# Kernel optimization log

Hardware: AMD Instinct MI355X
Metric: run time of the kernel (lower is better)

The kernel has to match this reference:

```python
import jax, jax.numpy as jnp
import numpy as np

N_LAYER = 3
N_HEAD = 12
D_K = 64
D_V = 64
D_MODEL = 768
D_INNER = 4096
LN_EPS = 1e-5
BN_EPS = 1e-5
PAD_ID = 1


def _layernorm(x, g, b):
    m = jnp.mean(x, axis=-1, keepdims=True)
    v = jnp.mean((x - m) ** 2, axis=-1, keepdims=True)
    return g * (x - m) / jnp.sqrt(v + LN_EPS) + b


def _batchnorm(x, g, b):
    # training-mode BatchNorm1d: per-feature batch statistics
    m = jnp.mean(x, axis=0)
    v = jnp.mean((x - m) ** 2, axis=0)
    return g * (x - m) / jnp.sqrt(v + BN_EPS) + b


def setup_inputs() -> dict:
    key = jax.random.key(0)
    ks = jax.random.split(key, 24)
    B, C, S, H = 4, 4, 256, D_MODEL
    inp = {
        'input_ids': jax.random.randint(ks[0], (B, C, S), 0, 50000, dtype=jnp.int64) if jax.config.read('jax_enable_x64') else jax.random.randint(ks[0], (B, C, S), 0, 50000, dtype=jnp.int32),
        'roberta_attn': jax.random.normal(ks[1], (B, C, S, H), dtype=jnp.float32),
        'pooled_output': jax.random.normal(ks[2], (B * C, H), dtype=jnp.float32),
        'commonsense_mask': jax.random.uniform(ks[3], (B, C, S, S), dtype=jnp.float32),
        'dependency_mask': jax.random.uniform(ks[4], (B, C, S, S), dtype=jnp.float32),
        'entity_mask': jax.random.uniform(ks[5], (B, C, S), dtype=jnp.float32),
        'sentiment_mask': jax.random.uniform(ks[6], (B, C, S, S), dtype=jnp.float32),
    }
    s = 0.02
    inp['lin_w'] = s * jax.random.normal(ks[7], (H, N_LAYER * 4), dtype=jnp.float32)
    inp['lin_b'] = jnp.zeros((N_LAYER * 4,), jnp.float32)
    inp['Wq'] = s * jax.random.normal(ks[8], (N_LAYER, H, N_HEAD * D_K), dtype=jnp.float32)
    inp['bq'] = jnp.zeros((N_LAYER, N_HEAD * D_K), jnp.float32)
    inp['Wk'] = s * jax.random.normal(ks[9], (N_LAYER, H, N_HEAD * D_K), dtype=jnp.float32)
    inp['bk'] = jnp.zeros((N_LAYER, N_HEAD * D_K), jnp.float32)
    inp['Wv'] = s * jax.random.normal(ks[10], (N_LAYER, H, N_HEAD * D_V), dtype=jnp.float32)
    inp['bv'] = jnp.zeros((N_LAYER, N_HEAD * D_V), jnp.float32)
    inp['Wo'] = s * jax.random.normal(ks[11], (N_LAYER, N_HEAD * D_V, H), dtype=jnp.float32)
    inp['bo'] = jnp.zeros((N_LAYER, H), jnp.float32)
    inp['ln1_g'] = jnp.ones((N_LAYER, H), jnp.float32)
    inp['ln1_b'] = jnp.zeros((N_LAYER, H), jnp.float32)
    inp['W1'] = s * jax.random.normal(ks[12], (N_LAYER, H, D_INNER), dtype=jnp.float32)
    inp['b1'] = jnp.zeros((N_LAYER, D_INNER), jnp.float32)
    inp['W2'] = s * jax.random.normal(ks[13], (N_LAYER, D_INNER, H), dtype=jnp.float32)
    inp['b2'] = jnp.zeros((N_LAYER, H), jnp.float32)
    inp['ln2_g'] = jnp.ones((N_LAYER, H), jnp.float32)
    inp['ln2_b'] = jnp.zeros((N_LAYER, H), jnp.float32)
    inp['bnt_g'] = jnp.ones((H,), jnp.float32)
    inp['bnt_b'] = jnp.zeros((H,), jnp.float32)
    inp['pool_w'] = s * jax.random.normal(ks[14], (H, H), dtype=jnp.float32)
    inp['pool_b'] = jnp.zeros((H,), jnp.float32)
    inp['bn_g'] = jnp.ones((H,), jnp.float32)
    inp['bn_b'] = jnp.zeros((H,), jnp.float32)
    inp['cls_w'] = s * jax.random.normal(ks[15], (H, 1), dtype=jnp.float32)
    inp['cls_b'] = jnp.zeros((1,), jnp.float32)
    return inp


def reference(input_ids, roberta_attn, pooled_output, commonsense_mask, dependency_mask,
              entity_mask, sentiment_mask, lin_w, lin_b, Wq, bq, Wk, bk, Wv, bv, Wo, bo,
              ln1_g, ln1_b, W1, b1, W2, b2, ln2_g, ln2_b, bnt_g, bnt_b,
              pool_w, pool_b, bn_g, bn_b, cls_w, cls_b):
    B, C, S = input_ids.shape
    H = roberta_attn.shape[-1]
    N = B * C
    x = roberta_attn.reshape(N, S, H)

    # learned softmax fusion weights over the 4 relational masks, per layer
    w = jnp.mean(x, axis=1) @ lin_w + lin_b                       # [N, 3*4]
    w = jax.nn.softmax(w.reshape(N, N_LAYER, 4).transpose(1, 0, 2), axis=-1)  # [3, N, 4]

    ent = jnp.broadcast_to(entity_mask[:, :, None, :], (B, C, S, S))
    masks = jnp.stack([
        commonsense_mask.reshape(N, S, S),
        dependency_mask.reshape(N, S, S),
        ent.reshape(N, S, S),
        sentiment_mask.reshape(N, S, S),
    ], axis=1)                                                     # [N, 4, S, S]
    bias = jnp.einsum('lnm,nmqk->lnqk', w, masks)                  # [3, N, S, S]

    non_pad = (input_ids.reshape(N, S) != PAD_ID).astype(x.dtype)[:, :, None]  # [N, S, 1]

    enc = x
    scale = 1.0 / np.sqrt(D_K).astype(np.float32)
    for l in range(N_LAYER):
        residual = enc
        q = (enc @ Wq[l] + bq[l]).reshape(N, S, N_HEAD, D_K)
        k = (enc @ Wk[l] + bk[l]).reshape(N, S, N_HEAD, D_K)
        v = (enc @ Wv[l] + bv[l]).reshape(N, S, N_HEAD, D_V)
        scores = jnp.einsum('nqhd,nkhd->nhqk', q, k) * scale + bias[l][:, None]  # [N,H,S,S]
        attn = jax.nn.softmax(scores, axis=-1)
        o = jnp.einsum('nhqk,nkhd->nqhd', attn, v).reshape(N, S, N_HEAD * D_V)
        o = o @ Wo[l] + bo[l]
        enc = _layernorm(o + residual, ln1_g[l], ln1_b[l]) * non_pad
        residual = enc
        f = jax.nn.relu(enc @ W1[l] + b1[l]) @ W2[l] + b2[l]
        enc = _layernorm(f + residual, ln2_g[l], ln2_b[l]) * non_pad

    enc = _batchnorm(enc.reshape(N * S, H), bnt_g, bnt_b).reshape(N, S, H)
    seq = x + enc
    pooled = jnp.tanh(seq[:, 0] @ pool_w + pool_b)
    pooled = _batchnorm(pooled, bn_g, bn_b)
    logits = pooled @ cls_w + cls_b                                # [N, 1]
    return logits.reshape(-1, C)
```

## Files before the change

kernel.cpp:

```cpp
#include <hip/hip_runtime.h>
#include <hip/hip_bf16.h>
#include <math.h>

#define NSEQ 16
#define SEQ 256
#define H 768
#define NH 12
#define DKH 64
#define DI 4096
#define MROWS (NSEQ*SEQ)
#define QKVN (3*H)

typedef __bf16 v8bf __attribute__((ext_vector_type(8)));
typedef float  v4f  __attribute__((ext_vector_type(4)));
typedef short  v8s  __attribute__((ext_vector_type(8)));

__device__ inline unsigned short bf16b(float f) {
  __hip_bfloat16 h = __float2bfloat16(f);
  return *reinterpret_cast<unsigned short*>(&h);
}
__device__ inline float b2f(unsigned short b) {
  return __uint_as_float(((unsigned int)b) << 16);
}

__device__ __forceinline__ void gload16(const void* g, void* l) {
  __builtin_amdgcn_global_load_lds((const __attribute__((address_space(1))) void*)g,
                                   (__attribute__((address_space(3))) void*)l, 16, 0, 0);
}

__device__ __forceinline__ void waitvm(int n) {
  switch (n) {
    case 0:  asm volatile("s_waitcnt vmcnt(0)" ::: "memory"); break;
    case 2:  asm volatile("s_waitcnt vmcnt(2)" ::: "memory"); break;
    case 4:  asm volatile("s_waitcnt vmcnt(4)" ::: "memory"); break;
    case 8:  asm volatile("s_waitcnt vmcnt(8)" ::: "memory"); break;
    case 12: asm volatile("s_waitcnt vmcnt(12)" ::: "memory"); break;
    case 16: asm volatile("s_waitcnt vmcnt(16)" ::: "memory"); break;
    default: asm volatile("s_waitcnt vmcnt(0)" ::: "memory"); break;
  }
}

enum { MODE_F32_BIAS=0, MODE_BF16_BIAS=1, MODE_BF16_BIAS_RELU=2, MODE_SCORES=3, MODE_PV=4, MODE_F32_NOBIAS=5 };

template<int BM, int BN, int MODE, int BK, int DEPTH, bool SWZ>
__global__ __launch_bounds__(256) void k_mm(
    const unsigned short* __restrict__ A, int lda, long long saN, long long saH,
    const unsigned short* __restrict__ B, int ldb, long long sbN, long long sbH,
    void* __restrict__ Cout, int ldc, long long scN, long long scH,
    const float* __restrict__ bias, int K, int nhdiv) {
  constexpr int MI = BM/32, NI = BN/32;
  constexpr int CH  = BK/8;
  constexpr int RPC = 512/BK;
  constexpr int SW  = CH - 1;
  constexpr int SSH = (BK == 32) ? 1 : 0;
  constexpr int AISS = BM*BK/2048, BISS = BN*BK/2048;
  constexpr int LPT = AISS + BISS;
  constexpr int TA = BM*BK, TB = BN*BK;
  __shared__ unsigned short As[DEPTH*TA];
  __shared__ unsigned short Bs[DEPTH*TB];
  int t = threadIdx.x;
  int z = blockIdx.z, n = z / nhdiv, h = z - n*nhdiv;
  int lane = t & 63, wid = t >> 6, wr = wid >> 1, wc = wid & 1;

  int bx = blockIdx.x, by = blockIdx.y;
  if (SWZ) {
    int gx = gridDim.x;
    int nwg = gx * gridDim.y;
    int lin = by*gx + bx;
    int q = nwg >> 3, r = nwg & 7;
    int xcd = lin & 7, idx = lin >> 3;
    int swz = (xcd < r) ? (xcd*(q+1) + idx) : (r*(q+1) + (xcd-r)*q + idx);
    bx = swz % gx; by = swz / gx;
  }

  const unsigned short* Ab = A + (size_t)n*saN + (size_t)h*saH + (size_t)by*BM*lda;
  const unsigned short* Bb = B + (size_t)n*sbN + (size_t)h*sbH + (size_t)bx*BN*ldb;

  const unsigned short* aSrc[AISS]; int aOff[AISS];
#pragma unroll
  for (int r = 0; r < AISS; ++r) {
    int chunk = wid*AISS + r;
    int row = chunk*RPC + lane/CH;
    int col = ((lane % CH) ^ ((row >> SSH) & SW)) * 8;
    aSrc[r] = Ab + (size_t)row*lda + col;
    aOff[r] = chunk*512;
  }
  const unsigned short* bSrc[BISS]; int bOff[BISS];
#pragma unroll
  for (int r = 0; r < BISS; ++r) {
    int chunk = wid*BISS + r;
    int row = chunk*RPC + lane/CH;
    int col = ((lane % CH) ^ ((row >> SSH) & SW)) * 8;
    bSrc[r] = Bb + (size_t)row*ldb + col;
    bOff[r] = chunk*512;
  }

  v4f acc[MI][NI];
#pragma unroll
  for (int i = 0; i < MI; ++i)
#pragma unroll
    for (int j = 0; j < NI; ++j) acc[i][j] = (v4f){0.f,0.f,0.f,0.f};

  auto issue = [&](int tt, int buf) {
    int k0 = tt * BK;
#pragma unroll
    for (int r = 0; r < AISS; ++r) gload16(aSrc[r] + k0, &As[buf*TA + aOff[r]]);
#pragma unroll
    for (int r = 0; r < BISS; ++r) gload16(bSrc[r] + k0, &Bs[buf*TB + bOff[r]]);
  };

  int nt = K / BK;
  for (int p = 0; p < DEPTH-1 && p < nt; ++p) issue(p, p);
  int cbuf = 0;
  int ibuf = (DEPTH-1) % DEPTH;
  for (int tt = 0; tt < nt; ++tt) {
    int ahead = tt + DEPTH - 1;
    if (ahead < nt) {
      issue(ahead, ibuf);
      waitvm((DEPTH-1)*LPT);
    } else {
      waitvm((nt-1-tt)*LPT);
    }
    __builtin_amdgcn_s_barrier();
    asm volatile("" ::: "memory");
#pragma unroll
    for (int ks = 0; ks < BK/32; ++ks) {
      v8bf af[MI], bfr[NI];
#pragma unroll
      for (int i = 0; i < MI; ++i) {
        int row = wr*(BM/2) + i*16 + (lane & 15);
        int c = (ks*4 + (lane >> 4)) ^ ((row >> SSH) & SW);
        af[i] = *(const v8bf*)&As[cbuf*TA + row*BK + c*8];
      }
#pragma unroll
      for (int j = 0; j < NI; ++j) {
        int row = wc*(BN/2) + j*16 + (lane & 15);
        int c = (ks*4 + (lane >> 4)) ^ ((row >> SSH) & SW);
        bfr[j] = *(const v8bf*)&Bs[cbuf*TB + row*BK + c*8];
      }
#pragma unroll
      for (int i = 0; i < MI; ++i)
#pragma unroll
        for (int j = 0; j < NI; ++j)
          acc[i][j] = __builtin_amdgcn_mfma_f32_16x16x32_bf16(af[i], bfr[j], acc[i][j], 0, 0, 0);
    }
    asm volatile("s_waitcnt lgkmcnt(0)" ::: "memory");
    __builtin_amdgcn_s_barrier();
    asm volatile("" ::: "memory");
    cbuf = (cbuf + 1 == DEPTH) ? 0 : cbuf + 1;
    ibuf = (ibuf + 1 == DEPTH) ? 0 : ibuf + 1;
  }

  float* Cf = (float*)Cout;
  unsigned short* Ch = (unsigned short*)Cout;
  size_t cb = (size_t)n*scN + (size_t)h*scH;
  int grow0 = by*BM + wr*(BM/2);
  int gcol0 = bx*BN + wc*(BN/2);
#pragma unroll
  for (int i = 0; i < MI; ++i) {
#pragma unroll
    for (int j = 0; j < NI; ++j) {
      int col = gcol0 + j*16 + (lane & 15);
      float bval = 0.f;
      if (MODE == MODE_F32_BIAS || MODE == MODE_BF16_BIAS || MODE == MODE_BF16_BIAS_RELU)
        bval = bias[col];
#pragma unroll
      for (int r = 0; r < 4; ++r) {
        int row = grow0 + i*16 + (lane>>4)*4 + r;
        float v = acc[i][j][r];
        if (MODE == MODE_F32_BIAS) {
          Cf[cb + (size_t)row*ldc + col] = v + bval;
        } else if (MODE == MODE_F32_NOBIAS) {
          Cf[cb + (size_t)row*ldc + col] = v;
        } else if (MODE == MODE_PV) {
          Ch[cb + (size_t)row*ldc + col] = bf16b(v);
        } else {
          v += bval;
          if (MODE == MODE_BF16_BIAS_RELU) v = fmaxf(v, 0.f);
          Ch[cb + (size_t)row*ldc + col] = bf16b(v);
        }
      }
    }
  }
}

template<int MODE>
__global__ __launch_bounds__(512) void k_mm256(
    const unsigned short* __restrict__ A, int lda,
    const unsigned short* __restrict__ B, int ldb,
    void* __restrict__ Cout, int ldc,
    const float* __restrict__ bias, int K) {
  extern __shared__ __align__(16) unsigned short smem[];
  unsigned short* As = smem;
  unsigned short* Bs = smem + 2*16384;
  constexpr int TA = 256*64;
  int t = threadIdx.x, lane = t & 63, wid = t >> 6;
  int wr = wid >> 2, wc = wid & 3;

  int bx = blockIdx.x, by = blockIdx.y;
  {
    int gx = gridDim.x, nwg = gx * gridDim.y;
    int lin = by*gx + bx;
    int q = nwg >> 3, r = nwg & 7;
    int xcd = lin & 7, idx = lin >> 3;
    int swz = (xcd < r) ? (xcd*(q+1) + idx) : (r*(q+1) + (xcd-r)*q + idx);
    bx = swz % gx; by = swz / gx;
  }

  const unsigned short* Ab = A + (size_t)by*256*lda;
  const unsigned short* Bb = B + (size_t)bx*256*ldb;

  const unsigned short* aSrc[4]; int aOff[4];
  const unsigned short* bSrc[4]; int bOff[4];
#pragma unroll
  for (int r = 0; r < 4; ++r) {
    int chunk = wid*4 + r;
    int row = chunk*8 + (lane >> 3);
    int col = ((lane & 7) ^ (row & 7)) * 8;
    aSrc[r] = Ab + (size_t)row*lda + col;
    bSrc[r] = Bb + (size_t)row*ldb + col;
    aOff[r] = chunk*512;
    bOff[r] = chunk*512;
  }

  v4f acc[8][4];
#pragma unroll
  for (int i = 0; i < 8; ++i)
#pragma unroll
    for (int j = 0; j < 4; ++j) acc[i][j] = (v4f){0.f,0.f,0.f,0.f};

  auto issue = [&](int tt, int buf) {
    int k0 = tt << 6;
#pragma unroll
    for (int r = 0; r < 4; ++r) gload16(aSrc[r] + k0, &As[buf*TA + aOff[r]]);
#pragma unroll
    for (int r = 0; r < 4; ++r) gload16(bSrc[r] + k0, &Bs[buf*TA + bOff[r]]);
  };

  int nt = K >> 6;
  issue(0, 0);
  int cur = 0;
  for (int tt = 0; tt < nt; ++tt) {
    if (tt + 1 < nt) {
      issue(tt+1, cur^1);
      waitvm(8);
    } else {
      waitvm(0);
    }
    __builtin_amdgcn_s_barrier();
    asm volatile("" ::: "memory");
    __builtin_amdgcn_s_setprio(1);
#pragma unroll
    for (int ks = 0; ks < 2; ++ks) {
      v8bf af[8], bfr[4];
#pragma unroll
      for (int i = 0; i < 8; ++i) {
        int row = wr*128 + i*16 + (lane & 15);
        int c = (ks*4 + (lane >> 4)) ^ (row & 7);
        af[i] = *(const v8bf*)&As[cur*TA + row*64 + c*8];
      }
#pragma unroll
      for (int j = 0; j < 4; ++j) {
        int row = wc*64 + j*16 + (lane & 15);
        int c = (ks*4 + (lane >> 4)) ^ (row & 7);
        bfr[j] = *(const v8bf*)&Bs[cur*TA + row*64 + c*8];
      }
#pragma unroll
      for (int i = 0; i < 8; ++i)
#pragma unroll
        for (int j = 0; j < 4; ++j)
          acc[i][j] = __builtin_amdgcn_mfma_f32_16x16x32_bf16(af[i], bfr[j], acc[i][j], 0, 0, 0);
    }
    __builtin_amdgcn_s_setprio(0);
    asm volatile("s_waitcnt lgkmcnt(0)" ::: "memory");
    __builtin_amdgcn_s_barrier();
    asm volatile("" ::: "memory");
    cur ^= 1;
  }

  float* Cf = (float*)Cout;
  unsigned short* Ch = (unsigned short*)Cout;
  int grow0 = by*256 + wr*128;
  int gcol0 = bx*256 + wc*64;
#pragma unroll
  for (int i = 0; i < 8; ++i) {
#pragma unroll
    for (int j = 0; j < 4; ++j) {
      int col = gcol0 + j*16 + (lane & 15);
      float bval = 0.f;
      if (MODE == MODE_F32_BIAS || MODE == MODE_BF16_BIAS || MODE == MODE_BF16_BIAS_RELU)
        bval = bias[col];
#pragma unroll
      for (int r = 0; r < 4; ++r) {
        int row = grow0 + i*16 + (lane>>4)*4 + r;
        float v = acc[i][j][r];
        if (MODE == MODE_F32_BIAS) {
          Cf[(size_t)row*ldc + col] = v + bval;
        } else if (MODE == MODE_F32_NOBIAS) {
          Cf[(size_t)row*ldc + col] = v;
        } else {
          v += bval;
          if (MODE == MODE_BF16_BIAS_RELU) v = fmaxf(v, 0.f);
          Ch[(size_t)row*ldc + col] = bf16b(v);
        }
      }
    }
  }
}

__global__ __launch_bounds__(256) void k_qksm(
    const unsigned short* __restrict__ qkv,
    const unsigned short* __restrict__ biasb,
    unsigned short* __restrict__ P) {
  __shared__ unsigned short Qs[64*64];
  __shared__ unsigned short Ks[256*64];
  int t = threadIdx.x, lane = t & 63, wid = t >> 6;
  int z = blockIdx.y, n = z / NH, h = z - n*NH;
  int m0 = blockIdx.x * 64;
  const unsigned short* Qb = qkv + (size_t)n*SEQ*QKVN + (size_t)h*DKH + (size_t)m0*QKVN;
  const unsigned short* Kb = qkv + (size_t)n*SEQ*QKVN + H + (size_t)h*DKH;
#pragma unroll
  for (int r = 0; r < 2; ++r) {
    int chunk = wid*2 + r;
    int row = chunk*8 + (lane >> 3);
    int col = ((lane & 7) ^ (row & 7)) * 8;
    gload16(Qb + (size_t)row*QKVN + col, &Qs[chunk*512]);
  }
#pragma unroll
  for (int r = 0; r < 8; ++r) {
    int chunk = wid*8 + r;
    int row = chunk*8 + (lane >> 3);
    int col = ((lane & 7) ^ (row & 7)) * 8;
    gload16(Kb + (size_t)row*QKVN + col, &Ks[chunk*512]);
  }
  __syncthreads();
  v4f acc[16];
#pragma unroll
  for (int j = 0; j < 16; ++j) acc[j] = (v4f){0.f,0.f,0.f,0.f};
#pragma unroll
  for (int ks = 0; ks < 2; ++ks) {
    int arow = wid*16 + (lane & 15);
    int ac = (ks*4 + (lane >> 4)) ^ (arow & 7);
    v8bf af = *(const v8bf*)&Qs[arow*64 + ac*8];
#pragma unroll
    for (int j = 0; j < 16; ++j) {
      int brow = j*16 + (lane & 15);
      int bc = (ks*4 + (lane >> 4)) ^ (brow & 7);
      v8bf bf = *(const v8bf*)&Ks[brow*64 + bc*8];
      acc[j] = __builtin_amdgcn_mfma_f32_16x16x32_bf16(af, bf, acc[j], 0, 0, 0);
    }
  }
  int col = lane & 15, quad = lane >> 4;
  const unsigned short* bb = biasb + (size_t)n*65536;
  float e[16][4];
  float rm[4] = {-1e30f, -1e30f, -1e30f, -1e30f};
#pragma unroll
  for (int r = 0; r < 4; ++r) {
    int row = m0 + wid*16 + quad*4 + r;
#pragma unroll
    for (int j = 0; j < 16; ++j) {
      float v = acc[j][r]*0.125f + b2f(bb[(size_t)row*256 + j*16 + col]);
      e[j][r] = v;
      rm[r] = fmaxf(rm[r], v);
    }
  }
#pragma unroll
  for (int r = 0; r < 4; ++r)
#pragma unroll
    for (int m = 1; m < 16; m <<= 1) rm[r] = fmaxf(rm[r], __shfl_xor(rm[r], m, 64));
  float rs[4] = {0.f, 0.f, 0.f, 0.f};
#pragma unroll
  for (int r = 0; r < 4; ++r)
#pragma unroll
    for (int j = 0; j < 16; ++j) {
      float ev = __expf(e[j][r] - rm[r]);
      e[j][r] = ev;
      rs[r] += ev;
    }
#pragma unroll
  for (int r = 0; r < 4; ++r) {
#pragma unroll
    for (int m = 1; m < 16; m <<= 1) rs[r] += __shfl_xor(rs[r], m, 64);
    rs[r] = 1.0f/rs[r];
  }
  unsigned short* Pz = P + (size_t)z*65536;
#pragma unroll
  for (int r = 0; r < 4; ++r) {
    int row = m0 + wid*16 + quad*4 + r;
#pragma unroll
    for (int j = 0; j < 16; ++j)
      Pz[(size_t)row*256 + j*16 + col] = bf16b(e[j][r]*rs[r]);
  }
}

__global__ __launch_bounds__(256) void k_wT(const float* __restrict__ in,
                                            unsigned short* __restrict__ out,
                                            int Nn, int Kk) {
  int n0 = blockIdx.x*64, k0 = blockIdx.y*64;
  __shared__ float T[64][72];
  int t = threadIdx.x;
  int r = t >> 4, c4 = (t & 15) * 4;
#pragma unroll
  for (int i = 0; i < 4; ++i) {
    float4 v = *(const float4*)(in + (size_t)(k0 + r + i*16)*Nn + n0 + c4);
    T[c4+0][r+i*16] = v.x; T[c4+1][r+i*16] = v.y;
    T[c4+2][r+i*16] = v.z; T[c4+3][r+i*16] = v.w;
  }
  __syncthreads();
  int c = t >> 3, r8 = (t & 7) * 8;
#pragma unroll
  for (int i = 0; i < 2; ++i) {
    int cc = c + i*32;
    v8s o;
#pragma unroll
    for (int j = 0; j < 8; ++j) o[j] = (short)bf16b(T[cc][r8+j]);
    *(v8s*)(out + (size_t)(n0+cc)*Kk + k0 + r8) = o;
  }
}

__global__ void k_bqkv(const float* __restrict__ bq, const float* __restrict__ bk,
                       const float* __restrict__ bv, float* __restrict__ o) {
  int i = blockIdx.x*256 + threadIdx.x;
  if (i >= 3*QKVN) return;
  int l = i / QKVN, j = i - l*QKVN;
  float v = (j < H) ? bq[l*H + j] : (j < 2*H) ? bk[l*H + j - H] : bv[l*H + j - 2*H];
  o[i] = v;
}

__global__ __launch_bounds__(256) void k_cast(const float* __restrict__ x,
                                              float* __restrict__ enc,
                                              unsigned short* __restrict__ enc16) {
  size_t i = ((size_t)blockIdx.x*256 + threadIdx.x)*4;
  float4 v = *(const float4*)(x + i);
  *(float4*)(enc + i) = v;
  ushort4 u = { bf16b(v.x), bf16b(v.y), bf16b(v.z), bf16b(v.w) };
  *(ushort4*)(enc16 + i) = u;
}

__global__ __launch_bounds__(256) void k_vT(const unsigned short* __restrict__ qkv,
                                            unsigned short* __restrict__ vT) {
  int z = blockIdx.x, n = z/NH, h = z - n*NH;
  const unsigned short* src = qkv + (size_t)n*SEQ*QKVN + 2*H + (size_t)h*DKH;
  __shared__ unsigned short tile[64][264];
  int t = threadIdx.x;
  int r0 = t >> 3, d0 = (t & 7) * 8;
#pragma unroll
  for (int i = 0; i < 8; ++i) {
    int r = r0 + i*32;
    v8s vv = *(const v8s*)(src + (size_t)r*QKVN + d0);
#pragma unroll
    for (int j = 0; j < 8; ++j) tile[d0+j][r] = (unsigned short)vv[j];
  }
  __syncthreads();
  int d = t >> 2, rb = (t & 3) * 64;
  unsigned short* dst = vT + (size_t)z*DKH*SEQ + (size_t)d*SEQ + rb;
#pragma unroll
  for (int i = 0; i < 8; ++i)
    *(v8s*)(dst + i*8) = *(const v8s*)&tile[d][rb + i*8];
}

__global__ __launch_bounds__(256) void k_fusion_weights(
    const float* __restrict__ x, const float* __restrict__ lin_w,
    const float* __restrict__ lin_b, float* __restrict__ wsoft) {
  int n = blockIdx.x, t = threadIdx.x;
  __shared__ float xm[H];
  __shared__ float sred[4];
  __shared__ float logits[12];
  if (t < 192) {
    const float4* p = (const float4*)(x + (size_t)n*SEQ*H) + t;
    float4 s = {0.f,0.f,0.f,0.f};
    for (int r = 0; r < SEQ; ++r) {
      float4 v = p[(size_t)r*192];
      s.x += v.x; s.y += v.y; s.z += v.z; s.w += v.w;
    }
    xm[t*4+0] = s.x*(1.0f/SEQ); xm[t*4+1] = s.y*(1.0f/SEQ);
    xm[t*4+2] = s.z*(1.0f/SEQ); xm[t*4+3] = s.w*(1.0f/SEQ);
  }
  __syncthreads();
  float lacc[12];
#pragma unroll
  for (int j = 0; j < 12; ++j) lacc[j] = 0.f;
  for (int hh = t; hh < H; hh += 256) {
    float xv = xm[hh];
#pragma unroll
    for (int j = 0; j < 12; ++j) lacc[j] += xv * lin_w[hh*12 + j];
  }
  for (int j = 0; j < 12; ++j) {
    float v = lacc[j];
#pragma unroll
    for (int m = 1; m < 64; m <<= 1) v += __shfl_xor(v, m, 64);
    if ((t & 63) == 0) sred[t >> 6] = v;
    __syncthreads();
    if (t == 0) logits[j] = sred[0]+sred[1]+sred[2]+sred[3] + lin_b[j];
    __syncthreads();
  }
  if (t < 3) {
    int l = t;
    float mx = -1e30f;
    for (int m = 0; m < 4; ++m) mx = fmaxf(mx, logits[l*4+m]);
    float e[4], s = 0.f;
    for (int m = 0; m < 4; ++m) { e[m] = expf(logits[l*4+m]-mx); s += e[m]; }
    for (int m = 0; m < 4; ++m) wsoft[(l*NSEQ + n)*4 + m] = e[m]/s;
  }
}

__global__ __launch_bounds__(256) void k_bias(
    const float* __restrict__ cm, const float* __restrict__ dm,
    const float* __restrict__ ent, const float* __restrict__ sm,
    const float* __restrict__ wsoft, int l, unsigned short* __restrict__ bias) {
  int g = blockIdx.x*256 + threadIdx.x;
  int n = g >> 14;
  int k4 = g & 63;
  const float* w = wsoft + (l*NSEQ + n)*4;
  float w0 = w[0], w1 = w[1], w2 = w[2], w3 = w[3];
  float4 c = ((const float4*)cm)[g];
  float4 d = ((const float4*)dm)[g];
  float4 s = ((const float4*)sm)[g];
  float4 e = ((const float4*)(ent + (size_t)n*SEQ))[k4];
  ushort4 o;
  o.x = bf16b(w0*c.x + w1*d.x + w2*e.x + w3*s.x);
  o.y = bf16b(w0*c.y + w1*d.y + w2*e.y + w3*s.y);
  o.z = bf16b(w0*c.z + w1*d.z + w2*e.z + w3*s.z);
  o.w = bf16b(w0*c.w + w1*d.w + w2*e.w + w3*s.w);
  ((ushort4*)bias)[g] = o;
}

__global__ void k_nonpad(const int* __restrict__ ids, float* __restrict__ npad) {
  int i = blockIdx.x*256 + threadIdx.x;
  if (i < MROWS) npad[i] = (ids[i] != 1) ? 1.0f : 0.0f;
}

__global__ __launch_bounds__(256) void k_ln(
    const float* __restrict__ f, float* __restrict__ enc,
    unsigned short* __restrict__ enc16,
    const float* __restrict__ g, const float* __restrict__ b,
    const float* __restrict__ npad) {
  int r = blockIdx.x, t = threadIdx.x;
  size_t base = (size_t)r*H;
  float v0 = f[base+t]     + enc[base+t];
  float v1 = f[base+t+256] + enc[base+t+256];
  float v2 = f[base+t+512] + enc[base+t+512];
  __shared__ float sred[4];
  float s = v0+v1+v2;
#pragma unroll
  for (int m = 1; m < 64; m <<= 1) s += __shfl_xor(s, m, 64);
  if ((t & 63) == 0) sred[t >> 6] = s;
  __syncthreads();
  float mean = (sred[0]+sred[1]+sred[2]+sred[3]) * (1.0f/H);
  __syncthreads();
  float d0 = v0-mean, d1 = v1-mean, d2 = v2-mean;
  float ss = d0*d0 + d1*d1 + d2*d2;
#pragma unroll
  for (int m = 1; m < 64; m <<= 1) ss += __shfl_xor(ss, m, 64);
  if ((t & 63) == 0) sred[t >> 6] = ss;
  __syncthreads();
  float var = (sred[0]+sred[1]+sred[2]+sred[3]) * (1.0f/H);
  float rstd = 1.0f/sqrtf(var + 1e-5f);
  float npv = npad[r];
  float o0 = (g[t]    *d0*rstd + b[t]    )*npv;
  float o1 = (g[t+256]*d1*rstd + b[t+256])*npv;
  float o2 = (g[t+512]*d2*rstd + b[t+512])*npv;
  enc[base+t]     = o0; enc[base+t+256] = o1; enc[base+t+512] = o2;
  enc16[base+t]     = bf16b(o0);
  enc16[base+t+256] = bf16b(o1);
  enc16[base+t+512] = bf16b(o2);
}

__global__ __launch_bounds__(256) void k_ln4(
    const float* __restrict__ p, float* __restrict__ enc,
    unsigned short* __restrict__ enc16,
    const float* __restrict__ g, const float* __restrict__ b,
    const float* __restrict__ npad, const float* __restrict__ cbias) {
  int r = blockIdx.x, t = threadIdx.x;
  size_t base = (size_t)r*H;
  const size_t PS = (size_t)MROWS*H;
  float v0 = p[base+t]     + p[PS+base+t]     + p[2*PS+base+t]     + p[3*PS+base+t]     + cbias[t]     + enc[base+t];
  float v1 = p[base+t+256] + p[PS+base+t+256] + p[2*PS+base+t+256] + p[3*PS+base+t+256] + cbias[t+256] + enc[base+t+256];
  float v2 = p[base+t+512] + p[PS+base+t+512] + p[2*PS+base+t+512] + p[3*PS+base+t+512] + cbias[t+512] + enc[base+t+512];
  __shared__ float sred[4];
  float s = v0+v1+v2;
#pragma unroll
  for (int m = 1; m < 64; m <<= 1) s += __shfl_xor(s, m, 64);
  if ((t & 63) == 0) sred[t >> 6] = s;
  __syncthreads();
  float mean = (sred[0]+sred[1]+sred[2]+sred[3]) * (1.0f/H);
  __syncthreads();
  float d0 = v0-mean, d1 = v1-mean, d2 = v2-mean;
  float ss = d0*d0 + d1*d1 + d2*d2;
#pragma unroll
  for (int m = 1; m < 64; m <<= 1) ss += __shfl_xor(ss, m, 64);
  if ((t & 63) == 0) sred[t >> 6] = ss;
  __syncthreads();
  float var = (sred[0]+sred[1]+sred[2]+sred[3]) * (1.0f/H);
  float rstd = 1.0f/sqrtf(var + 1e-5f);
  float npv = npad[r];
  float o0 = (g[t]    *d0*rstd + b[t]    )*npv;
  float o1 = (g[t+256]*d1*rstd + b[t+256])*npv;
  float o2 = (g[t+512]*d2*rstd + b[t+512])*npv;
  enc[base+t]     = o0; enc[base+t+256] = o1; enc[base+t+512] = o2;
  enc16[base+t]     = bf16b(o0);
  enc16[base+t+256] = bf16b(o1);
  enc16[base+t+512] = bf16b(o2);
}

__global__ __launch_bounds__(256) void k_colstats(
    const float* __restrict__ enc, float* __restrict__ csum, float* __restrict__ csq) {
  int r0 = blockIdx.x*16, t = threadIdx.x;
  float s0=0,s1=0,s2=0,q0=0,q1=0,q2=0;
  for (int r = 0; r < 16; ++r) {
    const float* row = enc + (size_t)(r0+r)*H;
    float a = row[t], b = row[t+256], c = row[t+512];
    s0 += a; s1 += b; s2 += c;
    q0 += a*a; q1 += b*b; q2 += c*c;
  }
  atomicAdd(&csum[t],     s0); atomicAdd(&csum[t+256], s1); atomicAdd(&csum[t+512], s2);
  atomicAdd(&csq[t],      q0); atomicAdd(&csq[t+256],  q1); atomicAdd(&csq[t+512],  q2);
}

__global__ __launch_bounds__(256) void k_poolprep(
    const float* __restrict__ x, const float* __restrict__ enc,
    const float* __restrict__ csum, const float* __restrict__ csq,
    const float* __restrict__ bnt_g, const float* __restrict__ bnt_b,
    float* __restrict__ ps0) {
  int n = blockIdx.x, t = threadIdx.x;
  for (int hh = t; hh < H; hh += 256) {
    float m = csum[hh] * (1.0f/MROWS);
    float var = csq[hh] * (1.0f/MROWS) - m*m;
    float rstd = 1.0f/sqrtf(var + 1e-5f);
    float e = enc[(size_t)n*SEQ*H + hh];
    ps0[n*H + hh] = x[(size_t)n*SEQ*H + hh] + bnt_g[hh]*(e-m)*rstd + bnt_b[hh];
  }
}

__global__ __launch_bounds__(256) void k_poolmm(
    const float* __restrict__ ps0, const float* __restrict__ pool_w,
    const float* __restrict__ pool_b, float* __restrict__ pooled) {
  int n = blockIdx.y, jb = blockIdx.x*64;
  __shared__ float s0[H];
  __shared__ float part[4][64];
  int t = threadIdx.x;
  for (int hh = t; hh < H; hh += 256) s0[hh] = ps0[n*H + hh];
  __syncthreads();
  int j = t & 63, q = t >> 6;
  float a = 0.f;
  int h0 = q*192;
  for (int hh = h0; hh < h0+192; ++hh)
    a = fmaf(s0[hh], pool_w[(size_t)hh*H + jb + j], a);
  part[q][j] = a;
  __syncthreads();
  if (t < 64) {
    float v = part[0][t]+part[1][t]+part[2][t]+part[3][t] + pool_b[jb+t];
    pooled[n*H + jb + t] = tanhf(v);
  }
}

__global__ __launch_bounds__(256) void k_final(
    const float* __restrict__ pooled, const float* __restrict__ bn_g,
    const float* __restrict__ bn_b, const float* __restrict__ cls_w,
    const float* __restrict__ cls_b, float* __restrict__ out) {
  int t = threadIdx.x;
  float acc[16];
#pragma unroll
  for (int n = 0; n < 16; ++n) acc[n] = 0.f;
  for (int hh = t; hh < H; hh += 256) {
    float p[16]; float m = 0.f;
#pragma unroll
    for (int n = 0; n < 16; ++n) { p[n] = pooled[n*H + hh]; m += p[n]; }
    m *= (1.0f/16.f);
    float var = 0.f;
#pragma unroll
    for (int n = 0; n < 16; ++n) { float d = p[n]-m; var += d*d; }
    var *= (1.0f/16.f);
    float rstd = 1.0f/sqrtf(var + 1e-5f);
    float gw = bn_g[hh]*rstd*cls_w[hh];
    float off = bn_b[hh]*cls_w[hh];
#pragma unroll
    for (int n = 0; n < 16; ++n) acc[n] += (p[n]-m)*gw + off;
  }
  __shared__ float sred[4];
  for (int n = 0; n < 16; ++n) {
    float v = acc[n];
#pragma unroll
    for (int m = 1; m < 64; m <<= 1) v += __shfl_xor(v, m, 64);
    if ((t & 63) == 0) sred[t >> 6] = v;
    __syncthreads();
    if (t == 0) out[n] = sred[0]+sred[1]+sred[2]+sred[3] + cls_b[0];
    __syncthreads();
  }
}

extern "C" void kernel_launch(void* const* d_in, const int* in_sizes, int n_in,
                              void* d_out, int out_size, void* d_ws, size_t ws_size,
                              hipStream_t stream) {
  const int*   input_ids = (const int*)  d_in[0];
  const float* x       = (const float*)d_in[1];
  const float* cm      = (const float*)d_in[3];
  const float* dm      = (const float*)d_in[4];
  const float* ent     = (const float*)d_in[5];
  const float* sm      = (const float*)d_in[6];
  const float* lin_w   = (const float*)d_in[7];
  const float* lin_b   = (const float*)d_in[8];
  const float* Wq      = (const float*)d_in[9];
  const float* bq      = (const float*)d_in[10];
  const float* Wk      = (const float*)d_in[11];
  const float* bk      = (const float*)d_in[12];
  const float* Wv      = (const float*)d_in[13];
  const float* bv      = (const float*)d_in[14];
  const float* Wo      = (const float*)d_in[15];
  const float* bo      = (const float*)d_in[16];
  const float* ln1_g   = (const float*)d_in[17];
  const float* ln1_b   = (const float*)d_in[18];
  const float* W1      = (const float*)d_in[19];
  const float* b1      = (const float*)d_in[20];
  const float* W2      = (const float*)d_in[21];
  const float* b2      = (const float*)d_in[22];
  const float* ln2_g   = (const float*)d_in[23];
  const float* ln2_b   = (const float*)d_in[24];
  const float* bnt_g   = (const float*)d_in[25];
  const float* bnt_b   = (const float*)d_in[26];
  const float* pool_w  = (const float*)d_in[27];
  const float* pool_b  = (const float*)d_in[28];
  const float* bn_g    = (const float*)d_in[29];
  const float* bn_b    = (const float*)d_in[30];
  const float* cls_w   = (const float*)d_in[31];
  const float* cls_b   = (const float*)d_in[32];
  float* out = (float*)d_out;
  (void)ws_size; (void)n_in; (void)in_sizes; (void)out_size;

  char* wsb = (char*)d_ws;
  size_t off = 0;
  auto alloc = [&](size_t bytes) {
    void* p = (void*)(wsb + off);
    off += (bytes + 255) & ~(size_t)255;
    return p;
  };
  float* enc            = (float*)alloc((size_t)MROWS*H*4);
  unsigned short* enc16 = (unsigned short*)alloc((size_t)MROWS*H*2);
  unsigned short* qkv16 = (unsigned short*)alloc((size_t)MROWS*QKVN*2);
  unsigned short* vT    = (unsigned short*)alloc((size_t)192*DKH*SEQ*2);
  unsigned short* ob16  = (unsigned short*)alloc((size_t)MROWS*H*2);
  float* fbuf           = (float*)alloc((size_t)4*MROWS*H*4);
  unsigned short* PH    = (unsigned short*)alloc((size_t)MROWS*DI*2);
  unsigned short* P16     = PH;
  unsigned short* hidden16 = PH;
  unsigned short* biasb = (unsigned short*)alloc((size_t)NSEQ*SEQ*SEQ*2);
  unsigned short* WqkvT = (unsigned short*)alloc((size_t)3*QKVN*H*2);
  unsigned short* WoT   = (unsigned short*)alloc((size_t)3*H*H*2);
  unsigned short* W1T   = (unsigned short*)alloc((size_t)3*DI*H*2);
  unsigned short* W2T   = (unsigned short*)alloc((size_t)3*H*DI*2);
  float* bqkv   = (float*)alloc(3*QKVN*4);
  float* wsoft  = (float*)alloc(3*16*4*4);
  float* npad   = (float*)alloc(MROWS*4);
  float* csum   = (float*)alloc(H*4);
  float* csq    = (float*)alloc(H*4);
  float* ps0    = (float*)alloc(16*H*4);
  float* pooled = (float*)alloc(16*H*4);

  k_cast<<<MROWS*H/1024, 256, 0, stream>>>(x, enc, enc16);
  k_fusion_weights<<<16, 256, 0, stream>>>(x, lin_w, lin_b, wsoft);
  k_nonpad<<<MROWS/256, 256, 0, stream>>>(input_ids, npad);
  k_bqkv<<<27, 256, 0, stream>>>(bq, bk, bv, bqkv);
  for (int l = 0; l < 3; ++l) {
    k_wT<<<dim3(12,12), 256, 0, stream>>>(Wq + (size_t)l*H*H, WqkvT + (size_t)l*QKVN*H,           H, H);
    k_wT<<<dim3(12,12), 256, 0, stream>>>(Wk + (size_t)l*H*H, WqkvT + (size_t)l*QKVN*H + H*H,     H, H);
    k_wT<<<dim3(12,12), 256, 0, stream>>>(Wv + (size_t)l*H*H, WqkvT + (size_t)l*QKVN*H + 2*H*H,   H, H);
    k_wT<<<dim3(12,12), 256, 0, stream>>>(Wo + (size_t)l*H*H, WoT + (size_t)l*H*H,                H, H);
    k_wT<<<dim3(64,12), 256, 0, stream>>>(W1 + (size_t)l*H*DI, W1T + (size_t)l*DI*H,              DI, H);
    k_wT<<<dim3(12,64), 256, 0, stream>>>(W2 + (size_t)l*DI*H, W2T + (size_t)l*H*DI,              H, DI);
  }

  for (int l = 0; l < 3; ++l) {
    k_bias<<<1024, 256, 0, stream>>>(cm, dm, ent, sm, wsoft, l, biasb);
    k_mm<128,128,MODE_BF16_BIAS,32,2,true><<<dim3(18,32,1), 256, 0, stream>>>(
        enc16, H, 0, 0, WqkvT + (size_t)l*QKVN*H, H, 0, 0,
        qkv16, QKVN, 0, 0, bqkv + l*QKVN, H, 1);
    k_qksm<<<dim3(4,192), 256, 0, stream>>>(qkv16, biasb, P16);
    k_vT<<<192, 256, 0, stream>>>(qkv16, vT);
    k_mm<64,64,MODE_PV,64,3,false><<<dim3(1,4,192), 256, 0, stream>>>(
        P16, SEQ, (long long)NH*SEQ*SEQ, (long long)SEQ*SEQ,
        vT, SEQ, (long long)NH*DKH*SEQ, (long long)DKH*SEQ,
        ob16, H, (long long)SEQ*H, DKH,
        nullptr, SEQ, NH);
    k_mm<64,64,MODE_F32_BIAS,64,3,true><<<dim3(12,64,1), 256, 0, stream>>>(
        ob16, H, 0, 0, WoT + (size_t)l*H*H, H, 0, 0,
        fbuf, H, 0, 0, bo + l*H, H, 1);
    k_ln<<<MROWS, 256, 0, stream>>>(fbuf, enc, enc16, ln1_g + l*H, ln1_b + l*H, npad);
    k_mm256<MODE_BF16_BIAS_RELU><<<dim3(16,16), 512, 131072, stream>>>(
        enc16, H, W1T + (size_t)l*DI*H, H, hidden16, DI, b1 + l*DI, H);
    k_mm<128,128,MODE_F32_NOBIAS,32,2,true><<<dim3(6,32,4), 256, 0, stream>>>(
        hidden16, DI, 0, 1024, W2T + (size_t)l*H*DI, DI, 0, 1024,
        fbuf, H, 0, (long long)MROWS*H, nullptr, 1024, 4);
    k_ln4<<<MROWS, 256, 0, stream>>>(fbuf, enc, enc16, ln2_g + l*H, ln2_b + l*H, npad, b2 + l*H);
  }

  hipMemsetAsync(csum, 0, H*sizeof(float), stream);
  hipMemsetAsync(csq,  0, H*sizeof(float), stream);
  k_colstats<<<256, 256, 0, stream>>>(enc, csum, csq);
  k_poolprep<<<16, 256, 0, stream>>>(x, enc, csum, csq, bnt_g, bnt_b, ps0);
  k_poolmm<<<dim3(12,16), 256, 0, stream>>>(ps0, pool_w, pool_b, pooled);
  k_final<<<1, 256, 0, stream>>>(pooled, bn_g, bn_b, cls_w, cls_b, out);
}
```

Measured before the change: 643.4 us.

## Interleave global prefetch with MFMA phases in 256x256 FFN1 GEMM

The 256-tile GEMM main loop is split into four sub-phases per k-tile. Each phase issues one slice of the next tile's global-to-LDS loads, then reads LDS fragments and runs half of the MFMA work, with explicit lgkmcnt waits and sched_barriers between phases. The goal is to spread memory issue across the compute instead of bursting it, with fewer live B fragments per phase. Separately, the Wo projection GEMM template parameters change (K-tile 64 to 32, stages 3 to 2). Risks include extra waits serializing LDS reads with MFMA, and a smaller K tile for Wo.

```diff
diff --git a/kernel.cpp b/kernel.cpp
--- a/kernel.cpp
+++ b/kernel.cpp
@@ -185,7 +185,7 @@
 }
 
 template<int MODE>
-__global__ __launch_bounds__(512) void k_mm256(
+__global__ __launch_bounds__(512) void k_mm256p8(
     const unsigned short* __restrict__ A, int lda,
     const unsigned short* __restrict__ B, int ldb,
     void* __restrict__ Cout, int ldc,
@@ -193,7 +193,7 @@
   extern __shared__ __align__(16) unsigned short smem[];
   unsigned short* As = smem;
   unsigned short* Bs = smem + 2*16384;
-  constexpr int TA = 256*64;
+  constexpr int TT = 256*64;
   int t = threadIdx.x, lane = t & 63, wid = t >> 6;
   int wr = wid >> 2, wc = wid & 3;
 
@@ -229,53 +229,57 @@
 #pragma unroll
     for (int j = 0; j < 4; ++j) acc[i][j] = (v4f){0.f,0.f,0.f,0.f};
 
-  auto issue = [&](int tt, int buf) {
+  auto issueAB = [&](int tt, int buf, int q) {
     int k0 = tt << 6;
-#pragma unroll
-    for (int r = 0; r < 4; ++r) gload16(aSrc[r] + k0, &As[buf*TA + aOff[r]]);
-#pragma unroll
-    for (int r = 0; r < 4; ++r) gload16(bSrc[r] + k0, &Bs[buf*TA + bOff[r]]);
+    gload16(aSrc[q] + k0, &As[buf*TT + aOff[q]]);
+    gload16(bSrc[q] + k0, &Bs[buf*TT + bOff[q]]);
   };
 
   int nt = K >> 6;
-  issue(0, 0);
-  int cur = 0;
+#pragma unroll
+  for (int q = 0; q < 4; ++q) issueAB(0, 0, q);
+
   for (int tt = 0; tt < nt; ++tt) {
-    if (tt + 1 < nt) {
-      issue(tt+1, cur^1);
-      waitvm(8);
-    } else {
-      waitvm(0);
-    }
-    __builtin_amdgcn_s_barrier();
-    asm volatile("" ::: "memory");
-    __builtin_amdgcn_s_setprio(1);
-#pragma unroll
-    for (int ks = 0; ks < 2; ++ks) {
-      v8bf af[8], bfr[4];
+    int cur = tt & 1, nxt = cur ^ 1;
+    bool more = (tt + 1 < nt);
+#pragma unroll
+    for (int q = 0; q < 4; ++q) {
+      if (q == 0) {
+        if (more) issueAB(tt+1, nxt, 0);
+        waitvm(more ? 2 : 0);
+        __builtin_amdgcn_s_barrier();
+        asm volatile("" ::: "memory");
+      } else {
+        if (more) issueAB(tt+1, nxt, q);
+      }
+      int ks = q & 1, jh = q >> 1;
+      v8bf af[8], bfr[2];
 #pragma unroll
       for (int i = 0; i < 8; ++i) {
         int row = wr*128 + i*16 + (lane & 15);
         int c = (ks*4 + (lane >> 4)) ^ (row & 7);
-        af[i] = *(const v8bf*)&As[cur*TA + row*64 + c*8];
+        af[i] = *(const v8bf*)&As[cur*TT + row*64 + c*8];
       }
 #pragma unroll
-      for (int j = 0; j < 4; ++j) {
-        int row = wc*64 + j*16 + (lane & 15);
+      for (int jj = 0; jj < 2; ++jj) {
+        int row = wc*64 + (jh*2 + jj)*16 + (lane & 15);
         int c = (ks*4 + (lane >> 4)) ^ (row & 7);
-        bfr[j] = *(const v8bf*)&Bs[cur*TA + row*64 + c*8];
+        bfr[jj] = *(const v8bf*)&Bs[cur*TT + row*64 + c*8];
       }
+      asm volatile("s_waitcnt lgkmcnt(0)" ::: "memory");
+      __builtin_amdgcn_sched_barrier(0);
+      __builtin_amdgcn_s_setprio(1);
 #pragma unroll
       for (int i = 0; i < 8; ++i)
 #pragma unroll
-        for (int j = 0; j < 4; ++j)
-          acc[i][j] = __builtin_amdgcn_mfma_f32_16x16x32_bf16(af[i], bfr[j], acc[i][j], 0, 0, 0);
+        for (int jj = 0; jj < 2; ++jj)
+          acc[i][jh*2+jj] = __builtin_amdgcn_mfma_f32_16x16x32_bf16(af[i], bfr[jj], acc[i][jh*2+jj], 0, 0, 0);
+      __builtin_amdgcn_s_setprio(0);
+      if (q == 3) {
+        __builtin_amdgcn_s_barrier();
+        asm volatile("" ::: "memory");
+      }
     }
-    __builtin_amdgcn_s_setprio(0);
-    asm volatile("s_waitcnt lgkmcnt(0)" ::: "memory");
-    __builtin_amdgcn_s_barrier();
-    asm volatile("" ::: "memory");
-    cur ^= 1;
   }
 
   float* Cf = (float*)Cout;
@@ -781,11 +785,11 @@
         vT, SEQ, (long long)NH*DKH*SEQ, (long long)DKH*SEQ,
         ob16, H, (long long)SEQ*H, DKH,
         nullptr, SEQ, NH);
-    k_mm<64,64,MODE_F32_BIAS,64,3,true><<<dim3(12,64,1), 256, 0, stream>>>(
+    k_mm<64,64,MODE_F32_BIAS,32,2,true><<<dim3(12,64,1), 256, 0, stream>>>(
         ob16, H, 0, 0, WoT + (size_t)l*H*H, H, 0, 0,
         fbuf, H, 0, 0, bo + l*H, H, 1);
     k_ln<<<MROWS, 256, 0, stream>>>(fbuf, enc, enc16, ln1_g + l*H, ln1_b + l*H, npad);
-    k_mm256<MODE_BF16_BIAS_RELU><<<dim3(16,16), 512, 131072, stream>>>(
+    k_mm256p8<MODE_BF16_BIAS_RELU><<<dim3(16,16), 512, 131072, stream>>>(
         enc16, H, W1T + (size_t)l*DI*H, H, hidden16, DI, b1 + l*DI, H);
     k_mm<128,128,MODE_F32_NOBIAS,32,2,true><<<dim3(6,32,4), 256, 0, stream>>>(
         hidden16, DI, 0, 1024, W2T + (size_t)l*H*DI, DI, 0, 1024,
```

New measurement: 655.1 us. Within noise of the previous version (+1.8%).

## Fuse QK softmax and PV matmul into single attention kernel

Applied to the files above, without the earlier changes.

Merges the score+softmax kernel and the separate P·V GEMM into one kernel that keeps the probability tile in shared memory and multiplies it by a V tile loaded alongside Q and K. This removes the round trip of the bf16 probability matrix through global memory and one kernel launch per layer. Shared memory per block grows to about 104 KB (Q, K, V and P tiles), which may reduce occupancy. The P-to-LDS store is followed by a waitcnt and sched barrier rather than a block barrier, so each wave must only read back the P rows it wrote itself.

```diff
diff --git a/kernel.cpp b/kernel.cpp
--- a/kernel.cpp
+++ b/kernel.cpp
@@ -308,17 +308,21 @@
   }
 }
 
-__global__ __launch_bounds__(256) void k_qksm(
+__global__ __launch_bounds__(256) void k_attn(
     const unsigned short* __restrict__ qkv,
+    const unsigned short* __restrict__ vT,
     const unsigned short* __restrict__ biasb,
-    unsigned short* __restrict__ P) {
+    unsigned short* __restrict__ O) {
   __shared__ unsigned short Qs[64*64];
   __shared__ unsigned short Ks[256*64];
+  __shared__ unsigned short Vs[64*256];
+  __shared__ unsigned short Ps[64*256];
   int t = threadIdx.x, lane = t & 63, wid = t >> 6;
   int z = blockIdx.y, n = z / NH, h = z - n*NH;
   int m0 = blockIdx.x * 64;
   const unsigned short* Qb = qkv + (size_t)n*SEQ*QKVN + (size_t)h*DKH + (size_t)m0*QKVN;
   const unsigned short* Kb = qkv + (size_t)n*SEQ*QKVN + H + (size_t)h*DKH;
+  const unsigned short* Vb = vT + (size_t)z*DKH*SEQ;
 #pragma unroll
   for (int r = 0; r < 2; ++r) {
     int chunk = wid*2 + r;
@@ -333,7 +337,15 @@
     int col = ((lane & 7) ^ (row & 7)) * 8;
     gload16(Kb + (size_t)row*QKVN + col, &Ks[chunk*512]);
   }
-  __syncthreads();
+#pragma unroll
+  for (int r = 0; r < 8; ++r) {
+    int chunk = wid*8 + r;
+    int row = chunk*2 + (lane >> 5);
+    int cc = lane & 31;
+    gload16(Vb + (size_t)row*SEQ + (size_t)((cc ^ (row & 7))*8), &Vs[chunk*512]);
+  }
+  __syncthreads();
+
   v4f acc[16];
 #pragma unroll
   for (int j = 0; j < 16; ++j) acc[j] = (v4f){0.f,0.f,0.f,0.f};
@@ -350,6 +362,7 @@
       acc[j] = __builtin_amdgcn_mfma_f32_16x16x32_bf16(af, bf, acc[j], 0, 0, 0);
     }
   }
+
   int col = lane & 15, quad = lane >> 4;
   const unsigned short* bb = biasb + (size_t)n*65536;
   float e[16][4];
@@ -383,13 +396,44 @@
     for (int m = 1; m < 16; m <<= 1) rs[r] += __shfl_xor(rs[r], m, 64);
     rs[r] = 1.0f/rs[r];
   }
-  unsigned short* Pz = P + (size_t)z*65536;
+
 #pragma unroll
   for (int r = 0; r < 4; ++r) {
-    int row = m0 + wid*16 + quad*4 + r;
-#pragma unroll
-    for (int j = 0; j < 16; ++j)
-      Pz[(size_t)row*256 + j*16 + col] = bf16b(e[j][r]*rs[r]);
+    int row = wid*16 + quad*4 + r;
+#pragma unroll
+    for (int j = 0; j < 16; ++j) {
+      int cc = j*2 + (col >> 3);
+      Ps[row*256 + ((cc ^ (row & 7))*8) + (col & 7)] = bf16b(e[j][r]*rs[r]);
+    }
+  }
+  asm volatile("s_waitcnt lgkmcnt(0)" ::: "memory");
+  __builtin_amdgcn_sched_barrier(0);
+
+  v4f po[4];
+#pragma unroll
+  for (int j = 0; j < 4; ++j) po[j] = (v4f){0.f,0.f,0.f,0.f};
+#pragma unroll
+  for (int kk = 0; kk < 8; ++kk) {
+    int arow = wid*16 + (lane & 15);
+    int c = kk*4 + (lane >> 4);
+    v8bf af = *(const v8bf*)&Ps[arow*256 + ((c ^ (arow & 7))*8)];
+#pragma unroll
+    for (int j = 0; j < 4; ++j) {
+      int brow = j*16 + (lane & 15);
+      v8bf bf = *(const v8bf*)&Vs[brow*256 + ((c ^ (brow & 7))*8)];
+      po[j] = __builtin_amdgcn_mfma_f32_16x16x32_bf16(af, bf, po[j], 0, 0, 0);
+    }
+  }
+
+  unsigned short* Ob = O + ((size_t)n*SEQ + m0)*H + (size_t)h*DKH;
+#pragma unroll
+  for (int j = 0; j < 4; ++j) {
+    int ocol = j*16 + (lane & 15);
+#pragma unroll
+    for (int r = 0; r < 4; ++r) {
+      int orow = wid*16 + quad*4 + r;
+      Ob[(size_t)orow*H + ocol] = bf16b(po[j][r]);
+    }
   }
 }
 
@@ -741,7 +785,6 @@
   unsigned short* ob16  = (unsigned short*)alloc((size_t)MROWS*H*2);
   float* fbuf           = (float*)alloc((size_t)4*MROWS*H*4);
   unsigned short* PH    = (unsigned short*)alloc((size_t)MROWS*DI*2);
-  unsigned short* P16     = PH;
   unsigned short* hidden16 = PH;
   unsigned short* biasb = (unsigned short*)alloc((size_t)NSEQ*SEQ*SEQ*2);
   unsigned short* WqkvT = (unsigned short*)alloc((size_t)3*QKVN*H*2);
@@ -774,13 +817,8 @@
     k_mm<128,128,MODE_BF16_BIAS,32,2,true><<<dim3(18,32,1), 256, 0, stream>>>(
         enc16, H, 0, 0, WqkvT + (size_t)l*QKVN*H, H, 0, 0,
         qkv16, QKVN, 0, 0, bqkv + l*QKVN, H, 1);
-    k_qksm<<<dim3(4,192), 256, 0, stream>>>(qkv16, biasb, P16);
     k_vT<<<192, 256, 0, stream>>>(qkv16, vT);
-    k_mm<64,64,MODE_PV,64,3,false><<<dim3(1,4,192), 256, 0, stream>>>(
-        P16, SEQ, (long long)NH*SEQ*SEQ, (long long)SEQ*SEQ,
-        vT, SEQ, (long long)NH*DKH*SEQ, (long long)DKH*SEQ,
-        ob16, H, (long long)SEQ*H, DKH,
-        nullptr, SEQ, NH);
+    k_attn<<<dim3(4,192), 256, 0, stream>>>(qkv16, vT, biasb, ob16);
     k_mm<64,64,MODE_F32_BIAS,64,3,true><<<dim3(12,64,1), 256, 0, stream>>>(
         ob16, H, 0, 0, WoT + (size_t)l*H*H, H, 0, 0,
         fbuf, H, 0, 0, bo + l*H, H, 1);
```

New measurement: 643.1 us. About the same (-0.0%).
